# Optimization experiments

Hardware: AMD Instinct MI355X
Metric: run time of the kernel (lower is better)

The kernel has to match this reference:

```python
import jax, jax.numpy as jnp
import numpy as np

N_HEADS = 16


def setup_inputs() -> dict:
    key = jax.random.key(0)
    ks = jax.random.split(key, 4)
    B, S, D = 2, 2048, 1024
    x = jax.random.normal(ks[0], (B, S, D), dtype=jnp.float32)
    scale = 1.0 / np.sqrt(D)
    Wq = jax.random.normal(ks[1], (D, D), dtype=jnp.float32) * scale
    Wk = jax.random.normal(ks[2], (D, D), dtype=jnp.float32) * scale
    Wv = jax.random.normal(ks[3], (D, D), dtype=jnp.float32) * scale
    bq = jnp.zeros((D,), jnp.float32)
    bk = jnp.zeros((D,), jnp.float32)
    bv = jnp.zeros((D,), jnp.float32)
    return {"x": x, "Wq": Wq, "bq": bq, "Wk": Wk, "bk": bk, "Wv": Wv, "bv": bv}


def _split_heads(t, n_heads):
    B, S, D = t.shape
    return t.reshape(B, S, n_heads, D // n_heads).transpose(0, 2, 1, 3)  # [B,H,S,hd]


def reference(x, Wq, bq, Wk, bk, Wv, bv):
    H = N_HEADS
    Q = _split_heads(x @ Wq + bq, H)
    K = _split_heads(x @ Wk + bk, H)
    V = _split_heads(x @ Wv + bv, H)
    head_size = Q.shape[-1]
    scores = jnp.einsum("bhqd,bhkd->bhqk", Q, K) / jnp.sqrt(jnp.float32(head_size))
    probs = jax.nn.softmax(scores, axis=-1)  # dropout p=0.01 -> identity in eval
    out = jnp.einsum("bhqk,bhkd->bhqd", probs, V)
    B, _, S, hd = out.shape
    return out.transpose(0, 2, 1, 3).reshape(B, S, H * hd)
```

## Files before the change

kernel.cpp:

```cpp
#include <hip/hip_runtime.h>
#include <hip/hip_bf16.h>

typedef __bf16 bf16x8 __attribute__((ext_vector_type(8)));
typedef __bf16 bf16x4 __attribute__((ext_vector_type(4)));
typedef float f32x4 __attribute__((ext_vector_type(4)));
typedef unsigned u32x2 __attribute__((ext_vector_type(2)));
typedef unsigned u32x4 __attribute__((ext_vector_type(4)));

#define B_ 2
#define S_ 2048
#define D_ 1024
#define H_ 16
#define HD_ 64
#define NT_ (S_ / 64)

__device__ inline void load_lds16(const __bf16* g, __bf16* l) {
  __builtin_amdgcn_global_load_lds(
      (const __attribute__((address_space(1))) void*)g,
      (__attribute__((address_space(3))) void*)l, 16, 0, 0);
}

__global__ __launch_bounds__(256) void prep(
    const float* __restrict__ X,
    const float* __restrict__ Wq, const float* __restrict__ Wk,
    const float* __restrict__ Wv,
    __bf16* __restrict__ Xb, __bf16* __restrict__ WT)
{
  const int z = blockIdx.z, t = threadIdx.x;
  if (z == 3) {
    size_t base = ((size_t)(blockIdx.y * 16 + blockIdx.x)) * 16384 + t * 4;
#pragma unroll
    for (int i = 0; i < 16; ++i) {
      size_t idx = base + (size_t)i * 1024;
      f32x4 v = *(const f32x4*)(X + idx);
      __bf16 o[4];
#pragma unroll
      for (int j = 0; j < 4; ++j) o[j] = (__bf16)v[j];
      *(ulong1*)(Xb + idx) = *(ulong1*)o;
    }
    return;
  }
  const float* W = (z == 0) ? Wq : (z == 1) ? Wk : Wv;
  __bf16* WTz = WT + (size_t)z * D_ * D_;
  const int k0 = blockIdx.y * 64, n0 = blockIdx.x * 64;

  __shared__ __bf16 T[64 * 72];
  {
    int kl = t >> 2, cg = (t & 3) * 16;
    const float* wp = W + (size_t)(k0 + kl) * D_ + n0 + cg;
    bf16x8 a, b;
#pragma unroll
    for (int j = 0; j < 4; ++j) { a[j] = (__bf16)wp[j];     a[4 + j] = (__bf16)wp[4 + j]; }
#pragma unroll
    for (int j = 0; j < 4; ++j) { b[j] = (__bf16)wp[8 + j]; b[4 + j] = (__bf16)wp[12 + j]; }
    *(bf16x8*)(T + kl * 72 + cg) = a;
    *(bf16x8*)(T + kl * 72 + cg + 8) = b;
  }
  __syncthreads();
  {
    int nl = t >> 2, kc = (t & 3) * 16;
    bf16x8 a, b;
#pragma unroll
    for (int j = 0; j < 8; ++j) a[j] = T[(kc + j) * 72 + nl];
#pragma unroll
    for (int j = 0; j < 8; ++j) b[j] = T[(kc + 8 + j) * 72 + nl];
    __bf16* op = WTz + (size_t)(n0 + nl) * D_ + k0 + kc;
    *(bf16x8*)(op) = a;
    *(bf16x8*)(op + 8) = b;
  }
}

__global__ __launch_bounds__(256) void qkv_gemm(
    const __bf16* __restrict__ Xb, const __bf16* __restrict__ WT,
    const float* __restrict__ bq, const float* __restrict__ bk,
    const float* __restrict__ bv,
    __bf16* __restrict__ Qw, __bf16* __restrict__ Kw, __bf16* __restrict__ VTw)
{
  const int z = blockIdx.z;
  const __bf16* Wz = WT + (size_t)z * D_ * D_;
  const float* bias = (z == 0) ? bq : (z == 1) ? bk : bv;
  __bf16* outp = (z == 0) ? Qw : (z == 1) ? Kw : VTw;
  const float mult = (z == 0) ? 0.125f * 1.44269504088896f : 1.0f;

  const int tid  = threadIdx.x;
  const int wave = tid >> 6, lane = tid & 63, ln = lane & 15, quad = lane >> 4;
  const int m0 = blockIdx.y * 128, n0 = blockIdx.x * 128;
  const int wm = (wave & 1) * 64, wn = (wave >> 1) * 64;

  __shared__ __bf16 Als[128 * 32];
  __shared__ __bf16 Bls[128 * 32];

  f32x4 acc[4][4] = {};

  for (int k0 = 0; k0 < D_; k0 += 32) {
    __syncthreads();
#pragma unroll
    for (int i = 0; i < 2; ++i) {
      int cb = wave * 128 + i * 64;
      int chunk = cb + lane;
      int row = chunk >> 2, c = chunk & 3;
      int gc = c ^ (row & 3);
      load_lds16(Xb + (size_t)(m0 + row) * D_ + k0 + gc * 8, Als + cb * 8);
      load_lds16(Wz + (size_t)(n0 + row) * D_ + k0 + gc * 8, Bls + cb * 8);
    }
    __syncthreads();

    bf16x8 af[4], bfr[4];
    const int dsw = (quad ^ (ln & 3)) * 8;
#pragma unroll
    for (int mt = 0; mt < 4; ++mt)
      af[mt] = *(const bf16x8*)(Als + (wm + mt * 16 + ln) * 32 + dsw);
#pragma unroll
    for (int nt = 0; nt < 4; ++nt)
      bfr[nt] = *(const bf16x8*)(Bls + (wn + nt * 16 + ln) * 32 + dsw);
#pragma unroll
    for (int mt = 0; mt < 4; ++mt)
#pragma unroll
      for (int nt = 0; nt < 4; ++nt)
        acc[mt][nt] = __builtin_amdgcn_mfma_f32_16x16x32_bf16(af[mt], bfr[nt], acc[mt][nt], 0, 0, 0);
  }

#pragma unroll
  for (int nt = 0; nt < 4; ++nt) {
    int n_g = n0 + wn + nt * 16 + ln;
    float bv_ = bias[n_g];
#pragma unroll
    for (int mt = 0; mt < 4; ++mt) {
      if (z < 2) {
#pragma unroll
        for (int r = 0; r < 4; ++r) {
          int m_g = m0 + wm + mt * 16 + quad * 4 + r;
          outp[(size_t)m_g * D_ + n_g] = (__bf16)((acc[mt][nt][r] + bv_) * mult);
        }
      } else {
        int m_g0 = m0 + wm + mt * 16 + quad * 4;
        bf16x4 v4;
#pragma unroll
        for (int r = 0; r < 4; ++r) v4[r] = (__bf16)(acc[mt][nt][r] + bv_);
        *(bf16x4*)(outp + (size_t)(m_g0 >> 11) * D_ * S_ + (size_t)n_g * S_ + (m_g0 & (S_ - 1))) = v4;
      }
    }
  }
}

__global__ __launch_bounds__(256) void attn(
    const __bf16* __restrict__ Q, const __bf16* __restrict__ K,
    const __bf16* __restrict__ VT, float* __restrict__ out)
{
  const int tid  = threadIdx.x;
  const int wave = tid >> 6, lane = tid & 63, ln = lane & 15, quad = lane >> 4;

  const int f = blockIdx.x;
  const int xcd = f & 7, g = f >> 3;
  const int bh = ((g & 3) << 3) | xcd;
  const int qt = g >> 2;
  const int b = bh >> 4, h = bh & 15;
  const int q0 = qt * 128 + wave * 32;

  const __bf16* Qbase = Q + (size_t)(b * S_ + q0) * D_ + h * HD_;
  bf16x8 qb[2][2];
#pragma unroll
  for (int nt = 0; nt < 2; ++nt)
#pragma unroll
    for (int ks = 0; ks < 2; ++ks)
      qb[nt][ks] = *(const bf16x8*)(Qbase + (size_t)(nt * 16 + ln) * D_ + ks * 32 + quad * 8);

  const __bf16* Kh = K + (size_t)b * S_ * D_ + h * HD_;
  const __bf16* Vh = VT + (size_t)(b * D_ + h * HD_) * S_;

  __shared__ __bf16 Kls[2][64 * 64];
  __shared__ __bf16 Vls[2][80 * 64];

  {
    bf16x8 ones;
#pragma unroll
    for (int j = 0; j < 8; ++j) ones[j] = (__bf16)1.0f;
    int buf = tid >> 7, rr = (tid >> 3) & 15, cc = tid & 7;
    *(bf16x8*)(&Vls[buf][(64 + rr) * 64 + cc * 8]) = ones;
  }

  f32x4 acc[2][5] = {};

  const int swl = ln & 7;

  bf16x8 kreg[2], vreg[2];
#pragma unroll
  for (int i = 0; i < 2; ++i) {
    int chunk = i * 256 + tid, row = chunk >> 3, cc = chunk & 7;
    kreg[i] = *(const bf16x8*)(Kh + (size_t)row * D_ + cc * 8);
    vreg[i] = *(const bf16x8*)(Vh + (size_t)row * S_ + cc * 8);
  }

  for (int kt = 0; kt < NT_; ++kt) {
    __bf16* Kb = Kls[kt & 1];
    __bf16* Vb = Vls[kt & 1];
#pragma unroll
    for (int i = 0; i < 2; ++i) {
      int chunk = i * 256 + tid, row = chunk >> 3, cc = chunk & 7;
      int sw = (cc ^ (row & 7)) * 8;
      *(bf16x8*)(Kb + row * 64 + sw) = kreg[i];
      *(bf16x8*)(Vb + row * 64 + sw) = vreg[i];
    }
    if (kt + 1 < NT_) {
#pragma unroll
      for (int i = 0; i < 2; ++i) {
        int chunk = i * 256 + tid, row = chunk >> 3, cc = chunk & 7;
        kreg[i] = *(const bf16x8*)(Kh + (size_t)((kt + 1) * 64 + row) * D_ + cc * 8);
        vreg[i] = *(const bf16x8*)(Vh + (size_t)row * S_ + (kt + 1) * 64 + cc * 8);
      }
    }
    __syncthreads();

    f32x4 st[4][2] = {};
    __builtin_amdgcn_s_setprio(1);
#pragma unroll
    for (int mt = 0; mt < 4; ++mt) {
#pragma unroll
      for (int ks = 0; ks < 2; ++ks) {
        bf16x8 ka = *(const bf16x8*)(Kb + (mt * 16 + ln) * 64 + ((ks * 4 + quad) ^ swl) * 8);
#pragma unroll
        for (int nt = 0; nt < 2; ++nt)
          st[mt][nt] = __builtin_amdgcn_mfma_f32_16x16x32_bf16(ka, qb[nt][ks], st[mt][nt], 0, 0, 0);
      }
    }
    __builtin_amdgcn_s_setprio(0);

    bf16x8 pa[2][2];
#pragma unroll
    for (int nt = 0; nt < 2; ++nt)
#pragma unroll
      for (int ks = 0; ks < 2; ++ks) {
        bf16x4 p0, p1;
#pragma unroll
        for (int r = 0; r < 4; ++r) {
          p0[r] = (__bf16)__builtin_amdgcn_exp2f(st[2 * ks + 0][nt][r]);
          p1[r] = (__bf16)__builtin_amdgcn_exp2f(st[2 * ks + 1][nt][r]);
        }
        u32x2 d0 = __builtin_bit_cast(u32x2, p0);
        u32x2 d1 = __builtin_bit_cast(u32x2, p1);
        unsigned a = d0[0], bw = d0[1], c = d1[0], e = d1[1];
        asm("v_permlane32_swap_b32 %0, %1" : "+v"(a), "+v"(c));
        asm("v_permlane16_swap_b32 %0, %1" : "+v"(a), "+v"(c));
        asm("v_permlane32_swap_b32 %0, %1" : "+v"(bw), "+v"(e));
        asm("v_permlane16_swap_b32 %0, %1" : "+v"(bw), "+v"(e));
        u32x4 w;
        w[0] = a; w[1] = bw; w[2] = c; w[3] = e;
        pa[nt][ks] = __builtin_bit_cast(bf16x8, w);
      }

    __builtin_amdgcn_s_setprio(1);
#pragma unroll
    for (int ks = 0; ks < 2; ++ks) {
#pragma unroll
      for (int dt = 0; dt < 5; ++dt) {
        int vrow = (dt < 4) ? dt * 16 + ln : 64 + ln;
        bf16x8 vb = *(const bf16x8*)(Vb + vrow * 64 + ((ks * 4 + quad) ^ swl) * 8);
#pragma unroll
        for (int nt = 0; nt < 2; ++nt)
          acc[nt][dt] = __builtin_amdgcn_mfma_f32_16x16x32_bf16(pa[nt][ks], vb, acc[nt][dt], 0, 0, 0);
      }
    }
    __builtin_amdgcn_s_setprio(0);
  }

#pragma unroll
  for (int nt = 0; nt < 2; ++nt)
#pragma unroll
    for (int r = 0; r < 4; ++r) {
      float li = 1.0f / acc[nt][4][r];
      float* op = out + (size_t)(b * S_ + q0 + nt * 16 + quad * 4 + r) * D_ + h * HD_;
#pragma unroll
      for (int dt = 0; dt < 4; ++dt)
        op[dt * 16 + ln] = acc[nt][dt][r] * li;
    }
}

extern "C" void kernel_launch(void* const* d_in, const int* in_sizes, int n_in,
                              void* d_out, int out_size, void* d_ws, size_t ws_size,
                              hipStream_t stream) {
  const float* X  = (const float*)d_in[0];
  const float* Wq = (const float*)d_in[1];
  const float* bq = (const float*)d_in[2];
  const float* Wk = (const float*)d_in[3];
  const float* bk = (const float*)d_in[4];
  const float* Wv = (const float*)d_in[5];
  const float* bv = (const float*)d_in[6];

  __bf16* Qw  = (__bf16*)d_ws;
  __bf16* Kw  = Qw  + (size_t)B_ * S_ * D_;
  __bf16* VTw = Kw  + (size_t)B_ * S_ * D_;
  __bf16* Xb  = VTw + (size_t)B_ * S_ * D_;
  __bf16* WT  = Xb  + (size_t)B_ * S_ * D_;
  float* out = (float*)d_out;

  prep<<<dim3(16, 16, 4), 256, 0, stream>>>(X, Wq, Wk, Wv, Xb, WT);
  qkv_gemm<<<dim3(8, 32, 3), 256, 0, stream>>>(Xb, WT, bq, bk, bv, Qw, Kw, VTw);
  attn<<<512, 256, 0, stream>>>(Qw, Kw, VTw, out);
}
```

Measured before the change: 166.4 us.

## Split attention KV range across two blocks with atomic accumulation and normalize pass

Splits the key/value loop of attention into two halves handled by separate blocks, doubling the grid to 1024 blocks. Partial outputs and row sums are accumulated with float atomics into a zeroed output and an lbuf buffer, and a new norm_out kernel divides by the row sum. The scheme relies on the scores having no max subtraction, so partial sums can simply be added. K/V staging also switches to direct global-to-LDS loads, and the ones column moves from LDS to a register constant. The cost is atomic traffic, an extra zeroing pass over the output, and an additional kernel launch.

```diff
diff --git a/kernel.cpp b/kernel.cpp
--- a/kernel.cpp
+++ b/kernel.cpp
@@ -13,6 +13,7 @@
 #define H_ 16
 #define HD_ 64
 #define NT_ (S_ / 64)
+#define KSPLIT_ 2
 
 __device__ inline void load_lds16(const __bf16* g, __bf16* l) {
   __builtin_amdgcn_global_load_lds(
@@ -24,7 +25,8 @@
     const float* __restrict__ X,
     const float* __restrict__ Wq, const float* __restrict__ Wk,
     const float* __restrict__ Wv,
-    __bf16* __restrict__ Xb, __bf16* __restrict__ WT)
+    __bf16* __restrict__ Xb, __bf16* __restrict__ WT,
+    float* __restrict__ outZ, float* __restrict__ lbuf)
 {
   const int z = blockIdx.z, t = threadIdx.x;
   if (z == 3) {
@@ -38,6 +40,15 @@
       for (int j = 0; j < 4; ++j) o[j] = (__bf16)v[j];
       *(ulong1*)(Xb + idx) = *(ulong1*)o;
     }
+    return;
+  }
+  if (z == 4) {
+    const int blk = blockIdx.y * 16 + blockIdx.x;
+    size_t base = (size_t)blk * 16384 + t * 4;
+    f32x4 zz = {0.f, 0.f, 0.f, 0.f};
+#pragma unroll
+    for (int i = 0; i < 16; ++i) *(f32x4*)(outZ + base + (size_t)i * 1024) = zz;
+    lbuf[blk * 256 + t] = 0.0f;
     return;
   }
   const float* W = (z == 0) ? Wq : (z == 1) ? Wk : Wv;
@@ -145,7 +156,8 @@
 
 __global__ __launch_bounds__(256) void attn(
     const __bf16* __restrict__ Q, const __bf16* __restrict__ K,
-    const __bf16* __restrict__ VT, float* __restrict__ out)
+    const __bf16* __restrict__ VT, float* __restrict__ outO,
+    float* __restrict__ lbuf)
 {
   const int tid  = threadIdx.x;
   const int wave = tid >> 6, lane = tid & 63, ln = lane & 15, quad = lane >> 4;
@@ -153,7 +165,8 @@
   const int f = blockIdx.x;
   const int xcd = f & 7, g = f >> 3;
   const int bh = ((g & 3) << 3) | xcd;
-  const int qt = g >> 2;
+  const int qt = (g >> 2) & 15;
+  const int half = g >> 6;
   const int b = bh >> 4, h = bh & 15;
   const int q0 = qt * 128 + wave * 32;
 
@@ -169,47 +182,36 @@
   const __bf16* Vh = VT + (size_t)(b * D_ + h * HD_) * S_;
 
   __shared__ __bf16 Kls[2][64 * 64];
-  __shared__ __bf16 Vls[2][80 * 64];
-
-  {
-    bf16x8 ones;
-#pragma unroll
-    for (int j = 0; j < 8; ++j) ones[j] = (__bf16)1.0f;
-    int buf = tid >> 7, rr = (tid >> 3) & 15, cc = tid & 7;
-    *(bf16x8*)(&Vls[buf][(64 + rr) * 64 + cc * 8]) = ones;
-  }
+  __shared__ __bf16 Vls[2][64 * 64];
+
+  bf16x8 vones;
+#pragma unroll
+  for (int j = 0; j < 8; ++j) vones[j] = (__bf16)1.0f;
 
   f32x4 acc[2][5] = {};
-
   const int swl = ln & 7;
-
-  bf16x8 kreg[2], vreg[2];
-#pragma unroll
-  for (int i = 0; i < 2; ++i) {
-    int chunk = i * 256 + tid, row = chunk >> 3, cc = chunk & 7;
-    kreg[i] = *(const bf16x8*)(Kh + (size_t)row * D_ + cc * 8);
-    vreg[i] = *(const bf16x8*)(Vh + (size_t)row * S_ + cc * 8);
-  }
-
-  for (int kt = 0; kt < NT_; ++kt) {
-    __bf16* Kb = Kls[kt & 1];
-    __bf16* Vb = Vls[kt & 1];
-#pragma unroll
-    for (int i = 0; i < 2; ++i) {
-      int chunk = i * 256 + tid, row = chunk >> 3, cc = chunk & 7;
-      int sw = (cc ^ (row & 7)) * 8;
-      *(bf16x8*)(Kb + row * 64 + sw) = kreg[i];
-      *(bf16x8*)(Vb + row * 64 + sw) = vreg[i];
-    }
-    if (kt + 1 < NT_) {
-#pragma unroll
-      for (int i = 0; i < 2; ++i) {
-        int chunk = i * 256 + tid, row = chunk >> 3, cc = chunk & 7;
-        kreg[i] = *(const bf16x8*)(Kh + (size_t)((kt + 1) * 64 + row) * D_ + cc * 8);
-        vreg[i] = *(const bf16x8*)(Vh + (size_t)row * S_ + (kt + 1) * 64 + cc * 8);
-      }
-    }
+  const int kt0 = half * (NT_ / KSPLIT_);
+
+#define STAGE(kt_, bi_)                                                        \
+  {                                                                            \
+    _Pragma("unroll")                                                          \
+    for (int i = 0; i < 2; ++i) {                                              \
+      int cb = i * 256 + wave * 64;                                            \
+      int chunk = cb + lane, row = chunk >> 3, cc = chunk & 7;                 \
+      int sc = (cc ^ (row & 7)) * 8;                                           \
+      load_lds16(Kh + (size_t)((kt_) * 64 + row) * D_ + sc, &Kls[bi_][cb * 8]);\
+      load_lds16(Vh + (size_t)row * S_ + (kt_) * 64 + sc, &Vls[bi_][cb * 8]);  \
+    }                                                                          \
+  }
+
+  STAGE(kt0, 0);
+
+  for (int ki = 0; ki < NT_ / KSPLIT_; ++ki) {
+    const int bi = ki & 1;
+    __bf16* Kb = Kls[bi];
+    __bf16* Vb = Vls[bi];
     __syncthreads();
+    if (ki + 1 < NT_ / KSPLIT_) STAGE(kt0 + ki + 1, bi ^ 1);
 
     f32x4 st[4][2] = {};
     __builtin_amdgcn_s_setprio(1);
@@ -253,8 +255,9 @@
     for (int ks = 0; ks < 2; ++ks) {
 #pragma unroll
       for (int dt = 0; dt < 5; ++dt) {
-        int vrow = (dt < 4) ? dt * 16 + ln : 64 + ln;
-        bf16x8 vb = *(const bf16x8*)(Vb + vrow * 64 + ((ks * 4 + quad) ^ swl) * 8);
+        bf16x8 vb = (dt < 4)
+            ? *(const bf16x8*)(Vb + (dt * 16 + ln) * 64 + ((ks * 4 + quad) ^ swl) * 8)
+            : vones;
 #pragma unroll
         for (int nt = 0; nt < 2; ++nt)
           acc[nt][dt] = __builtin_amdgcn_mfma_f32_16x16x32_bf16(pa[nt][ks], vb, acc[nt][dt], 0, 0, 0);
@@ -262,17 +265,39 @@
     }
     __builtin_amdgcn_s_setprio(0);
   }
+#undef STAGE
 
 #pragma unroll
   for (int nt = 0; nt < 2; ++nt)
 #pragma unroll
     for (int r = 0; r < 4; ++r) {
-      float li = 1.0f / acc[nt][4][r];
-      float* op = out + (size_t)(b * S_ + q0 + nt * 16 + quad * 4 + r) * D_ + h * HD_;
+      int qrow = q0 + nt * 16 + quad * 4 + r;
+      float* op = outO + (size_t)(b * S_ + qrow) * D_ + h * HD_;
 #pragma unroll
       for (int dt = 0; dt < 4; ++dt)
-        op[dt * 16 + ln] = acc[nt][dt][r] * li;
-    }
+        atomicAdd(op + dt * 16 + ln, acc[nt][dt][r]);
+      if (ln == 0)
+        atomicAdd(lbuf + ((size_t)bh << 11) + qrow, acc[nt][4][r]);
+    }
+}
+
+__global__ __launch_bounds__(256) void norm_out(
+    float* __restrict__ outO, const float* __restrict__ lbuf)
+{
+  const int t = threadIdx.x;
+  const int sl = t >> 6;
+  const int d0 = (t & 63) * 16;
+  const int row = blockIdx.x * 4 + sl;
+  const int b = row >> 11, s = row & (S_ - 1);
+  const int h = d0 >> 6;
+  const float li = 1.0f / lbuf[(((size_t)((b << 4) | h)) << 11) + s];
+  float* p = outO + (size_t)row * D_ + d0;
+#pragma unroll
+  for (int j = 0; j < 4; ++j) {
+    f32x4 v = *(f32x4*)(p + j * 4);
+    v *= li;
+    *(f32x4*)(p + j * 4) = v;
+  }
 }
 
 extern "C" void kernel_launch(void* const* d_in, const int* in_sizes, int n_in,
@@ -291,9 +316,11 @@
   __bf16* VTw = Kw  + (size_t)B_ * S_ * D_;
   __bf16* Xb  = VTw + (size_t)B_ * S_ * D_;
   __bf16* WT  = Xb  + (size_t)B_ * S_ * D_;
+  float*  lbuf = (float*)(WT + (size_t)3 * D_ * D_);
   float* out = (float*)d_out;
 
-  prep<<<dim3(16, 16, 4), 256, 0, stream>>>(X, Wq, Wk, Wv, Xb, WT);
+  prep<<<dim3(16, 16, 5), 256, 0, stream>>>(X, Wq, Wk, Wv, Xb, WT, out, lbuf);
   qkv_gemm<<<dim3(8, 32, 3), 256, 0, stream>>>(Xb, WT, bq, bk, bv, Qw, Kw, VTw);
-  attn<<<512, 256, 0, stream>>>(Qw, Kw, VTw, out);
-}
+  attn<<<1024, 256, 0, stream>>>(Qw, Kw, VTw, out, lbuf);
+  norm_out<<<1024, 256, 0, stream>>>(out, lbuf);
+}
```

New measurement: 192.2 us. +15.5%, slower.

## Load K/V MFMA fragments directly from global into registers, dropping LDS staging

Applied to the files above, without the earlier changes.

The attention kernel no longer stages K and V tiles through double-buffered shared memory with barriers. Each wave now loads its own K and V MFMA operand fragments from global memory into registers, prefetching the next tile after each matmul phase, and supplies the row-sum ones column as a constant register. This removes LDS writes, reads and __syncthreads. In exchange, each of the four waves in a block refetches the same K/V data from global/L2, which multiplies memory traffic, and register pressure goes up.

```diff
diff --git a/kernel.cpp b/kernel.cpp
--- a/kernel.cpp
+++ b/kernel.cpp
@@ -165,65 +165,46 @@
     for (int ks = 0; ks < 2; ++ks)
       qb[nt][ks] = *(const bf16x8*)(Qbase + (size_t)(nt * 16 + ln) * D_ + ks * 32 + quad * 8);
 
-  const __bf16* Kh = K + (size_t)b * S_ * D_ + h * HD_;
-  const __bf16* Vh = VT + (size_t)(b * D_ + h * HD_) * S_;
-
-  __shared__ __bf16 Kls[2][64 * 64];
-  __shared__ __bf16 Vls[2][80 * 64];
-
-  {
-    bf16x8 ones;
-#pragma unroll
-    for (int j = 0; j < 8; ++j) ones[j] = (__bf16)1.0f;
-    int buf = tid >> 7, rr = (tid >> 3) & 15, cc = tid & 7;
-    *(bf16x8*)(&Vls[buf][(64 + rr) * 64 + cc * 8]) = ones;
-  }
+  const __bf16* kp = K + (size_t)b * S_ * D_ + h * HD_ + (size_t)ln * D_ + quad * 8;
+  const __bf16* vp = VT + (size_t)(b * D_ + h * HD_ + ln) * S_ + quad * 8;
+
+  bf16x8 vones;
+#pragma unroll
+  for (int j = 0; j < 8; ++j) vones[j] = (__bf16)1.0f;
 
   f32x4 acc[2][5] = {};
 
-  const int swl = ln & 7;
-
-  bf16x8 kreg[2], vreg[2];
-#pragma unroll
-  for (int i = 0; i < 2; ++i) {
-    int chunk = i * 256 + tid, row = chunk >> 3, cc = chunk & 7;
-    kreg[i] = *(const bf16x8*)(Kh + (size_t)row * D_ + cc * 8);
-    vreg[i] = *(const bf16x8*)(Vh + (size_t)row * S_ + cc * 8);
-  }
+  bf16x8 kf[4][2], vf[4][2];
+#pragma unroll
+  for (int mt = 0; mt < 4; ++mt)
+#pragma unroll
+    for (int ks = 0; ks < 2; ++ks)
+      kf[mt][ks] = *(const bf16x8*)(kp + (size_t)(mt * 16) * D_ + ks * 32);
+#pragma unroll
+  for (int dt = 0; dt < 4; ++dt)
+#pragma unroll
+    for (int ks = 0; ks < 2; ++ks)
+      vf[dt][ks] = *(const bf16x8*)(vp + (size_t)(dt * 16) * S_ + ks * 32);
 
   for (int kt = 0; kt < NT_; ++kt) {
-    __bf16* Kb = Kls[kt & 1];
-    __bf16* Vb = Vls[kt & 1];
-#pragma unroll
-    for (int i = 0; i < 2; ++i) {
-      int chunk = i * 256 + tid, row = chunk >> 3, cc = chunk & 7;
-      int sw = (cc ^ (row & 7)) * 8;
-      *(bf16x8*)(Kb + row * 64 + sw) = kreg[i];
-      *(bf16x8*)(Vb + row * 64 + sw) = vreg[i];
-    }
-    if (kt + 1 < NT_) {
-#pragma unroll
-      for (int i = 0; i < 2; ++i) {
-        int chunk = i * 256 + tid, row = chunk >> 3, cc = chunk & 7;
-        kreg[i] = *(const bf16x8*)(Kh + (size_t)((kt + 1) * 64 + row) * D_ + cc * 8);
-        vreg[i] = *(const bf16x8*)(Vh + (size_t)row * S_ + (kt + 1) * 64 + cc * 8);
-      }
-    }
-    __syncthreads();
-
     f32x4 st[4][2] = {};
     __builtin_amdgcn_s_setprio(1);
 #pragma unroll
-    for (int mt = 0; mt < 4; ++mt) {
-#pragma unroll
-      for (int ks = 0; ks < 2; ++ks) {
-        bf16x8 ka = *(const bf16x8*)(Kb + (mt * 16 + ln) * 64 + ((ks * 4 + quad) ^ swl) * 8);
+    for (int mt = 0; mt < 4; ++mt)
+#pragma unroll
+      for (int ks = 0; ks < 2; ++ks)
 #pragma unroll
         for (int nt = 0; nt < 2; ++nt)
-          st[mt][nt] = __builtin_amdgcn_mfma_f32_16x16x32_bf16(ka, qb[nt][ks], st[mt][nt], 0, 0, 0);
-      }
-    }
+          st[mt][nt] = __builtin_amdgcn_mfma_f32_16x16x32_bf16(kf[mt][ks], qb[nt][ks], st[mt][nt], 0, 0, 0);
     __builtin_amdgcn_s_setprio(0);
+
+    if (kt + 1 < NT_) {
+#pragma unroll
+      for (int mt = 0; mt < 4; ++mt)
+#pragma unroll
+        for (int ks = 0; ks < 2; ++ks)
+          kf[mt][ks] = *(const bf16x8*)(kp + (size_t)((kt + 1) * 64 + mt * 16) * D_ + ks * 32);
+    }
 
     bf16x8 pa[2][2];
 #pragma unroll
@@ -250,17 +231,23 @@
 
     __builtin_amdgcn_s_setprio(1);
 #pragma unroll
-    for (int ks = 0; ks < 2; ++ks) {
+    for (int ks = 0; ks < 2; ++ks)
 #pragma unroll
       for (int dt = 0; dt < 5; ++dt) {
-        int vrow = (dt < 4) ? dt * 16 + ln : 64 + ln;
-        bf16x8 vb = *(const bf16x8*)(Vb + vrow * 64 + ((ks * 4 + quad) ^ swl) * 8);
+        bf16x8 vb = (dt < 4) ? vf[dt][ks] : vones;
 #pragma unroll
         for (int nt = 0; nt < 2; ++nt)
           acc[nt][dt] = __builtin_amdgcn_mfma_f32_16x16x32_bf16(pa[nt][ks], vb, acc[nt][dt], 0, 0, 0);
       }
-    }
     __builtin_amdgcn_s_setprio(0);
+
+    if (kt + 1 < NT_) {
+#pragma unroll
+      for (int dt = 0; dt < 4; ++dt)
+#pragma unroll
+        for (int ks = 0; ks < 2; ++ks)
+          vf[dt][ks] = *(const bf16x8*)(vp + (size_t)(dt * 16) * S_ + (kt + 1) * 64 + ks * 32);
+    }
   }
 
 #pragma unroll
```

New measurement: 232.4 us. +39.6%, slower.
